# Performance work log

Measured on AMD Instinct MI355X. Metric: run time of the kernel, lower is better.

## Reference

```python
import jax, jax.numpy as jnp
import numpy as np

BETA = 0.5  # exp-sum normalization exponent (not a true softmax)


def setup_inputs() -> dict:
    key = jax.random.key(0)
    ks = jax.random.split(key, 12)
    b, h = 1024, 200
    item_num, region_num, user_num = 50000, 1000, 10000
    d, hid = 128, 128  # embed_size == hidden_size (required by the bmm reshape)
    std = 0.01
    return {
        "history": jax.random.randint(ks[0], (1, b, h), 0, item_num),
        "target": jax.random.randint(ks[1], (1, b), 0, item_num),
        "history_region": jax.random.randint(ks[2], (1, b, h), 0, region_num),
        "target_region": jax.random.randint(ks[3], (1, b), 0, region_num),
        "history_visit_rate": jax.random.uniform(ks[4], (1, h), dtype=jnp.float32),
        "dist_mat": jax.random.uniform(ks[5], (b, h), dtype=jnp.float32),
        "uid": 7,
        "embed_target": std * jax.random.normal(ks[6], (item_num, d // 2), dtype=jnp.float32),
        "embed_region": std * jax.random.normal(ks[7], (region_num, d // 2), dtype=jnp.float32),
        "embed_dist": std * jax.random.normal(ks[8], (user_num, region_num), dtype=jnp.float32),
        "Wq": jax.random.normal(ks[9], (hid, d), dtype=jnp.float32) * (1.0 / np.sqrt(d)),
        "Wk": jax.random.normal(ks[10], (hid, d), dtype=jnp.float32) * (1.0 / np.sqrt(d)),
        "Wv": jax.random.normal(ks[11], (d, d), dtype=jnp.float32) * (1.0 / np.sqrt(d)),
    }


def reference(history, target, history_region, target_region, history_visit_rate,
              dist_mat, uid, embed_target, embed_region, embed_dist, Wq, Wk, Wv):
    h_idx = history[0]            # [b, h]
    tgt = target[0]               # [b]
    hr = history_region[0]        # [b, h]
    tr = target_region[0]         # [b]
    hv = history_visit_rate[0]    # [h]
    b, hlen = h_idx.shape

    # embedding gathers + concat (target half | region half)
    hist_emb = jnp.concatenate([embed_target[h_idx], embed_region[hr]], axis=-1)  # [b,h,d]
    tgt_emb = jnp.concatenate([embed_target[tgt], embed_region[tr]], axis=-1)     # [b,d]
    hd = embed_dist[uid][hr]      # [b, h]
    td = embed_dist[uid][tr]      # [b]
    d = tgt_emb.shape[1]

    # QKV projections (torch Linear: y = x @ W.T)
    q = tgt_emb @ Wq.T            # [b, d]  (hidden == d)
    k = hist_emb @ Wk.T           # [b, h, d]
    v = hist_emb @ Wv.T           # [b, h, d]

    # faithful to original: key reshaped (NOT transposed) to [b, d, h]
    k_r = k.reshape(b, d, hlen)
    scores = jnp.einsum('bd,bdh->bh', q, k_r) / jnp.sqrt(jnp.float32(d))  # [b,h]

    # exp / beta-normalized attention with equality mask
    mask = (h_idx != tgt[:, None]).astype(scores.dtype)
    exp_A = jnp.exp(scores) * mask                          # [b,h]
    exp_sum = jnp.sum(exp_A, axis=-1) ** BETA               # [b]
    attn = exp_A / exp_sum[:, None]                         # [b,h]

    # geo weights: td @ hd is a vector-matrix product -> [h], broadcast over b
    geo = jnp.exp(-1.0 / (jax.nn.relu(td @ hd) + 1.0) * dist_mat)  # [b,h]

    result1 = v * (attn + geo)[..., None]                   # [b,h,d]
    result2 = hist_emb * jnp.broadcast_to(hv, (b, hlen))[..., None]
    result = result1 + result2                              # [b,h,d]

    pred = jnp.einsum('bhd,bd->b', result, tgt_emb)         # bmm + sum over h
    return jax.nn.sigmoid(pred)
```

## Files before the change

kernel.cpp:

```cpp
#include <hip/hip_runtime.h>

typedef unsigned short USH;
typedef unsigned int   UIN;
typedef unsigned char  UCH;

static constexpr int Bn = 1024;
static constexpr int Hn = 200;
static constexpr int Dn = 128;
static constexpr int Dh = 64;
static constexpr int NITEM = 50000;
static constexpr int NREG  = 1000;
static constexpr int MT = 64;
static constexpr int AB_A_BLOCKS = (NITEM + MT - 1) / MT;
static constexpr int AB_B_BLOCKS = (NREG  + MT - 1) / MT;
static constexpr int AB_TOT = AB_A_BLOCKS + AB_B_BLOCKS;
static constexpr int QU_BLOCKS = Bn / 4;
static constexpr int G_BLOCKS  = Bn / 16;
static constexpr int WTS = 132;
static constexpr int ETS = 69;
static constexpr int CR  = 50;
static constexpr int RS  = 192;

static constexpr float FSCALE = 128.f;
static constexpr float FINV   = 1.f / 128.f;

__device__ __forceinline__ float bf2f(USH u) {
  return __uint_as_float(((UIN)u) << 16);
}
__device__ __forceinline__ USH f2b(float f) {
  UIN x = __float_as_uint(f);
  return (USH)((x + 0x7fffu + ((x >> 16) & 1u)) >> 16);
}
__device__ __forceinline__ UIN enc4(float a, float b, float c, float d) {
  int w = __builtin_amdgcn_cvt_pk_fp8_f32(a, b, 0, false);
  w = __builtin_amdgcn_cvt_pk_fp8_f32(c, d, w, true);
  return (UIN)w;
}
__device__ __forceinline__ void dec4(UIN w, float* o) {
  auto lo = __builtin_amdgcn_cvt_pk_f32_fp8((int)w, false);
  auto hi = __builtin_amdgcn_cvt_pk_f32_fp8((int)w, true);
  o[0] = lo[0]; o[1] = lo[1]; o[2] = hi[0]; o[3] = hi[1];
}

__global__ __launch_bounds__(256, 2) void ab_kernel(
    const float* __restrict__ Et, const float* __restrict__ Er,
    const float* __restrict__ Wk, const float* __restrict__ Wq,
    const float* __restrict__ Wv, const int* __restrict__ target,
    const int* __restrict__ tregion, const int* __restrict__ hregion,
    const float* __restrict__ embed_dist, const int* __restrict__ uid,
    UCH* __restrict__ Cf, UCH* __restrict__ Df,
    float* __restrict__ qvt, float* __restrict__ uvt, float* __restrict__ g) {
  __shared__ float wt[64 * WTS];
  __shared__ float et[MT * ETS];
  int blk = blockIdx.x, tid = threadIdx.x;

  if (blk >= AB_TOT + QU_BLOCKS) {
    int c = tid;
    const float* row = embed_dist + (size_t)uid[0] * NREG;
    float acc = 0.f;
    int ibase = (blk - AB_TOT - QU_BLOCKS) * 16;
    for (int ii = 0; ii < 16; ii++) {
      int i = ibase + ii;
      float td = row[tregion[i]];
      if (c < Hn) acc += td * row[hregion[(size_t)i * Hn + c]];
    }
    if (c < Hn) atomicAdd(&g[c], acc);
    return;
  }

  if (blk >= AB_TOT) {
    float* te = wt;
    int i0 = (blk - AB_TOT) * 4;
#pragma unroll
    for (int v = 0; v < 2; v++) {
      int idx = v * 256 + tid;
      int ii = idx >> 7, d = idx & 127;
      int it = i0 + ii;
      te[ii * 128 + d] = (d < 64) ? Et[(size_t)target[it] * Dh + d]
                                  : Er[(size_t)tregion[it] * Dh + (d - 64)];
    }
    __syncthreads();
    int j = tid & 127, half = tid >> 7;
    float a0 = 0.f, a1 = 0.f, a2 = 0.f, a3 = 0.f;
    if (half == 0) {
      const float* wr = Wq + (size_t)j * Dn;
#pragma unroll 8
      for (int k = 0; k < 128; k++) {
        float w = wr[k];
        a0 += w * te[k]; a1 += w * te[128 + k];
        a2 += w * te[256 + k]; a3 += w * te[384 + k];
      }
      const float s = 0.088388347648318447f;
      qvt[(size_t)(i0 + 0) * Dn + j] = a0 * s;
      qvt[(size_t)(i0 + 1) * Dn + j] = a1 * s;
      qvt[(size_t)(i0 + 2) * Dn + j] = a2 * s;
      qvt[(size_t)(i0 + 3) * Dn + j] = a3 * s;
    } else {
      int d = j;
#pragma unroll 8
      for (int k = 0; k < 128; k++) {
        float w = Wv[(size_t)k * Dn + d];
        a0 += w * te[k]; a1 += w * te[128 + k];
        a2 += w * te[256 + k]; a3 += w * te[384 + k];
      }
      uvt[(size_t)(i0 + 0) * Dn + d] = a0;
      uvt[(size_t)(i0 + 1) * Dn + d] = a1;
      uvt[(size_t)(i0 + 2) * Dn + d] = a2;
      uvt[(size_t)(i0 + 3) * Dn + d] = a3;
    }
    return;
  }

  const float* E; UCH* OutT; int nmax, base, koff;
  if (blk < AB_A_BLOCKS) { E = Et; OutT = Cf; nmax = NITEM; base = blk * MT; koff = 0; }
  else { E = Er; OutT = Df; nmax = NREG; base = (blk - AB_A_BLOCKS) * MT; koff = 64; }

#pragma unroll
  for (int p = 0; p < 8; p++) {
    int idx = p * 256 + tid;
    int row = idx >> 4, c4 = idx & 15;
    float4 w = *reinterpret_cast<const float4*>(Wk + (size_t)row * Dn + koff + c4 * 4);
    wt[(c4 * 4 + 0) * WTS + row] = w.x;
    wt[(c4 * 4 + 1) * WTS + row] = w.y;
    wt[(c4 * 4 + 2) * WTS + row] = w.z;
    wt[(c4 * 4 + 3) * WTS + row] = w.w;
  }
#pragma unroll
  for (int p = 0; p < 4; p++) {
    int idx = p * 256 + tid;
    int m = idx >> 4, c4 = idx & 15;
    int gi = base + m;
    float4 e = make_float4(0.f, 0.f, 0.f, 0.f);
    if (gi < nmax) e = *reinterpret_cast<const float4*>(E + (size_t)gi * Dh + c4 * 4);
    et[m * ETS + c4 * 4 + 0] = e.x;
    et[m * ETS + c4 * 4 + 1] = e.y;
    et[m * ETS + c4 * 4 + 2] = e.z;
    et[m * ETS + c4 * 4 + 3] = e.w;
  }
  __syncthreads();

#pragma unroll
  for (int p = 0; p < 4; p++) {
    int idx = p * 256 + tid;
    int m = idx >> 4, wr = idx & 15;
    int gi = base + m;
    if (gi < nmax) {
      const float* er = &et[m * ETS + wr * 4];
      *reinterpret_cast<UIN*>(OutT + (size_t)gi * RS + 128 + wr * 4) =
          enc4(er[0] * FSCALE, er[1] * FSCALE, er[2] * FSCALE, er[3] * FSCALE);
    }
  }

  int jt = tid & 15, it = tid >> 4;
  const float* wb = wt + jt * 8;
  const float* eb = et + (it * 4) * ETS;
  float c[4][8];
#pragma unroll
  for (int ii = 0; ii < 4; ii++)
#pragma unroll
    for (int jj = 0; jj < 8; jj++) c[ii][jj] = 0.f;

#pragma unroll 2
  for (int k = 0; k < 64; k++) {
    float4 w0 = *reinterpret_cast<const float4*>(wb + (size_t)k * WTS);
    float4 w1 = *reinterpret_cast<const float4*>(wb + (size_t)k * WTS + 4);
    float e0 = eb[k], e1 = eb[ETS + k], e2 = eb[2 * ETS + k], e3 = eb[3 * ETS + k];
    c[0][0] += e0 * w0.x; c[0][1] += e0 * w0.y; c[0][2] += e0 * w0.z; c[0][3] += e0 * w0.w;
    c[0][4] += e0 * w1.x; c[0][5] += e0 * w1.y; c[0][6] += e0 * w1.z; c[0][7] += e0 * w1.w;
    c[1][0] += e1 * w0.x; c[1][1] += e1 * w0.y; c[1][2] += e1 * w0.z; c[1][3] += e1 * w0.w;
    c[1][4] += e1 * w1.x; c[1][5] += e1 * w1.y; c[1][6] += e1 * w1.z; c[1][7] += e1 * w1.w;
    c[2][0] += e2 * w0.x; c[2][1] += e2 * w0.y; c[2][2] += e2 * w0.z; c[2][3] += e2 * w0.w;
    c[2][4] += e2 * w1.x; c[2][5] += e2 * w1.y; c[2][6] += e2 * w1.z; c[2][7] += e2 * w1.w;
    c[3][0] += e3 * w0.x; c[3][1] += e3 * w0.y; c[3][2] += e3 * w0.z; c[3][3] += e3 * w0.w;
    c[3][4] += e3 * w1.x; c[3][5] += e3 * w1.y; c[3][6] += e3 * w1.z; c[3][7] += e3 * w1.w;
  }

#pragma unroll
  for (int ii = 0; ii < 4; ii++) {
    int item = base + it * 4 + ii;
    if (item < nmax) {
      uint2 pk;
      pk.x = enc4(c[ii][0] * FSCALE, c[ii][1] * FSCALE, c[ii][2] * FSCALE, c[ii][3] * FSCALE);
      pk.y = enc4(c[ii][4] * FSCALE, c[ii][5] * FSCALE, c[ii][6] * FSCALE, c[ii][7] * FSCALE);
      *reinterpret_cast<uint2*>(OutT + (size_t)item * RS + jt * 8) = pk;
    }
  }
}

__global__ __launch_bounds__(256, 6) void sc_kernel(
    const int* __restrict__ history, const int* __restrict__ target,
    const int* __restrict__ hregion, const int* __restrict__ tregion,
    const float* __restrict__ Et, const float* __restrict__ Er,
    const float* __restrict__ qvt, const float* __restrict__ uvt,
    const UCH* __restrict__ Cf, const UCH* __restrict__ Df,
    float* __restrict__ psc, float2* __restrict__ s12) {
  __shared__ USH kvs[CR * Dn];
  __shared__ uint4 rawA[CR * 4];
  __shared__ uint4 rawB[CR * 4];
  __shared__ float tgtE[128], uvf[128], qv[32];
  int b = blockIdx.x, i = b >> 2, h = b & 3;
  int tid = threadIdx.x;
  const int* hrow = history + (size_t)i * Hn + CR * h;
  const int* rrow = hregion + (size_t)i * Hn + CR * h;

  if (tid < 128) {
    tgtE[tid] = FINV * ((tid < 64) ? Et[(size_t)target[i] * Dh + tid]
                                   : Er[(size_t)tregion[i] * Dh + (tid - 64)]);
  } else {
    uvf[tid - 128] = FINV * uvt[(size_t)i * Dn + (tid - 128)];
  }
  if (tid < 32) qv[tid] = FINV * qvt[(size_t)i * Dn + 32 * h + tid];

  {
    int seg = tid & 3, row = tid >> 2;
    if (row < CR) {
      int ia = hrow[row], ib = rrow[row];
      rawA[row * 4 + seg] = *reinterpret_cast<const uint4*>(Cf + (size_t)ia * RS + 128 + seg * 16);
      rawB[row * 4 + seg] = *reinterpret_cast<const uint4*>(Df + (size_t)ib * RS + 128 + seg * 16);
    }
  }

#pragma unroll
  for (int p = 0; p < 2; p++) {
    int idx = p * 256 + tid;
    int seg = idx & 7, row = idx >> 3;
    if (row < CR) {
      int ia = hrow[row], ib = rrow[row];
      uint4 av = *reinterpret_cast<const uint4*>(Cf + (size_t)ia * RS + seg * 16);
      uint4 bv = *reinterpret_cast<const uint4*>(Df + (size_t)ib * RS + seg * 16);
      float fa[16], fb[16];
      dec4(av.x, fa);      dec4(av.y, fa + 4);  dec4(av.z, fa + 8);  dec4(av.w, fa + 12);
      dec4(bv.x, fb);      dec4(bv.y, fb + 4);  dec4(bv.z, fb + 8);  dec4(bv.w, fb + 12);
      uint4 k0, k1;
      k0.x = (UIN)f2b(fa[0] + fb[0])  | ((UIN)f2b(fa[1] + fb[1]) << 16);
      k0.y = (UIN)f2b(fa[2] + fb[2])  | ((UIN)f2b(fa[3] + fb[3]) << 16);
      k0.z = (UIN)f2b(fa[4] + fb[4])  | ((UIN)f2b(fa[5] + fb[5]) << 16);
      k0.w = (UIN)f2b(fa[6] + fb[6])  | ((UIN)f2b(fa[7] + fb[7]) << 16);
      k1.x = (UIN)f2b(fa[8] + fb[8])  | ((UIN)f2b(fa[9] + fb[9]) << 16);
      k1.y = (UIN)f2b(fa[10] + fb[10]) | ((UIN)f2b(fa[11] + fb[11]) << 16);
      k1.z = (UIN)f2b(fa[12] + fb[12]) | ((UIN)f2b(fa[13] + fb[13]) << 16);
      k1.w = (UIN)f2b(fa[14] + fb[14]) | ((UIN)f2b(fa[15] + fb[15]) << 16);
      *reinterpret_cast<uint4*>(&kvs[row * Dn + seg * 16]) = k0;
      *reinterpret_cast<uint4*>(&kvs[row * Dn + seg * 16 + 8]) = k1;
    }
  }
  __syncthreads();

  int l8 = tid & 7, r8 = tid >> 3;
#pragma unroll
  for (int pass = 0; pass < 2; pass++) {
    int t = (pass == 0) ? r8 : 32 + r8;
    if (t < CR) {
      uint2 e = *(reinterpret_cast<const uint2*>(&rawA[t * 4]) + l8);
      uint2 r = *(reinterpret_cast<const uint2*>(&rawB[t * 4]) + l8);
      float fe[8], fr[8];
      dec4(e.x, fe); dec4(e.y, fe + 4);
      dec4(r.x, fr); dec4(r.y, fr + 4);
      const float* u0 = &uvf[l8 * 8];       const float* t0 = &tgtE[l8 * 8];
      const float* u1 = &uvf[64 + l8 * 8];  const float* t1 = &tgtE[64 + l8 * 8];
      float s1a = fe[0] * u0[0] + fe[1] * u0[1] + fe[2] * u0[2] + fe[3] * u0[3]
                + fe[4] * u0[4] + fe[5] * u0[5] + fe[6] * u0[6] + fe[7] * u0[7]
                + fr[0] * u1[0] + fr[1] * u1[1] + fr[2] * u1[2] + fr[3] * u1[3]
                + fr[4] * u1[4] + fr[5] * u1[5] + fr[6] * u1[6] + fr[7] * u1[7];
      float s2a = fe[0] * t0[0] + fe[1] * t0[1] + fe[2] * t0[2] + fe[3] * t0[3]
                + fe[4] * t0[4] + fe[5] * t0[5] + fe[6] * t0[6] + fe[7] * t0[7]
                + fr[0] * t1[0] + fr[1] * t1[1] + fr[2] * t1[2] + fr[3] * t1[3]
                + fr[4] * t1[4] + fr[5] * t1[5] + fr[6] * t1[6] + fr[7] * t1[7];
      s1a += __shfl_xor(s1a, 1, 64); s2a += __shfl_xor(s2a, 1, 64);
      s1a += __shfl_xor(s1a, 2, 64); s2a += __shfl_xor(s2a, 2, 64);
      s1a += __shfl_xor(s1a, 4, 64); s2a += __shfl_xor(s2a, 4, 64);
      if (l8 == 0) s12[(size_t)i * Hn + CR * h + t] = make_float2(s1a, s2a);
    }
  }

  if (tid < Hn) {
    float acc = 0.f;
    const USH* kp = &kvs[tid];
#pragma unroll
    for (int a = 0; a < 32; a++) acc += qv[a] * bf2f(kp[a * 200]);
    psc[((size_t)i * 4 + h) * Hn + tid] = acc;
  }
}

__global__ __launch_bounds__(256, 8) void ep_kernel(
    const int* __restrict__ history, const int* __restrict__ target,
    const float* __restrict__ hv, const float* __restrict__ dist_mat,
    const float* __restrict__ g, const float* __restrict__ psc,
    const float2* __restrict__ s12, float* __restrict__ out) {
  __shared__ float red[8];
  int i = blockIdx.x, tid = threadIdx.x, lane = tid & 63, wave = tid >> 6;
  int tgt_i = target[i];

  float ea = 0.f; float2 sv = make_float2(0.f, 0.f);
  if (tid < Hn) {
    const float* pp = psc + (size_t)i * 4 * Hn + tid;
    float s = (pp[0] + pp[Hn]) + (pp[2 * Hn] + pp[3 * Hn]);
    sv = s12[(size_t)i * Hn + tid];
    ea = (history[(size_t)i * Hn + tid] != tgt_i) ? __expf(s) : 0.f;
  }
  float wsum = ea;
  for (int off = 32; off > 0; off >>= 1) wsum += __shfl_down(wsum, off, 64);
  if (lane == 0) red[wave] = wsum;
  __syncthreads();
  float esum = red[0] + red[1] + red[2] + red[3];
  float inv = esum > 0.f ? 1.f / sqrtf(esum) : 0.f;

  float part = 0.f;
  if (tid < Hn) {
    float gc = g[tid]; gc = gc > 0.f ? gc : 0.f;
    float dm = dist_mat[(size_t)i * Hn + tid];
    float geo = __expf(-dm / (gc + 1.f));
    part = (ea * inv + geo) * sv.x + hv[tid] * sv.y;
  }
  __syncthreads();
  for (int off = 32; off > 0; off >>= 1) part += __shfl_down(part, off, 64);
  if (lane == 0) red[wave] = part;
  __syncthreads();
  if (tid == 0) {
    float pred = red[0] + red[1] + red[2] + red[3];
    out[i] = 1.f / (1.f + __expf(-pred));
  }
}

extern "C" void kernel_launch(void* const* d_in, const int* in_sizes, int n_in,
                              void* d_out, int out_size, void* d_ws, size_t ws_size,
                              hipStream_t stream) {
  const int*   history = (const int*)d_in[0];
  const int*   target  = (const int*)d_in[1];
  const int*   hregion = (const int*)d_in[2];
  const int*   tregion = (const int*)d_in[3];
  const float* hv      = (const float*)d_in[4];
  const float* dist    = (const float*)d_in[5];
  const int*   uid     = (const int*)d_in[6];
  const float* Et      = (const float*)d_in[7];
  const float* Er      = (const float*)d_in[8];
  const float* Edist   = (const float*)d_in[9];
  const float* Wq      = (const float*)d_in[10];
  const float* Wk      = (const float*)d_in[11];
  const float* Wv      = (const float*)d_in[12];

  char* w = (char*)d_ws;
  float* g   = (float*)w;
  UCH*   Cf  = (UCH*)(w + 1024);
  UCH*   Df  = Cf + (size_t)NITEM * RS;
  float* qvt = (float*)(Df + (size_t)NREG * RS);
  float* uvt = qvt + (size_t)Bn * Dn;
  float* psc = uvt + (size_t)Bn * Dn;
  float2* s12 = (float2*)(psc + (size_t)Bn * 4 * Hn);
  float* out = (float*)d_out;

  hipMemsetAsync(g, 0, Hn * sizeof(float), stream);
  ab_kernel<<<AB_TOT + QU_BLOCKS + G_BLOCKS, 256, 0, stream>>>(
      Et, Er, Wk, Wq, Wv, target, tregion, hregion, Edist, uid,
      Cf, Df, qvt, uvt, g);
  sc_kernel<<<Bn * 4, 256, 0, stream>>>(history, target, hregion, tregion,
                                        Et, Er, qvt, uvt, Cf, Df, psc, s12);
  ep_kernel<<<Bn, 256, 0, stream>>>(history, target, hv, dist, g, psc, s12, out);
}
```

Before: 152.2 us.

## Fuse three kernels into one persistent cooperative kernel with grid syncs

Merges the projection/table-building, scoring, and epilogue kernels into one cooperative persistent kernel. Each block loops over virtual block indices, and grid.sync() separates the phases. The aim is to drop two kernel launch gaps and their tail effects. In exchange, the grid is capped at occupancy times 256 CUs, shared memory is sized for the largest phase (which may limit occupancy in later phases), and grid-wide barriers add their own cost.

New measurement: 291.6 us. 1.92x slower.

```diff
diff --git a/kernel.cpp b/kernel.cpp
--- a/kernel.cpp
+++ b/kernel.cpp
@@ -1,4 +1,7 @@
 #include <hip/hip_runtime.h>
+#include <hip/hip_cooperative_groups.h>
+
+namespace cg = cooperative_groups;
 
 typedef unsigned short USH;
 typedef unsigned int   UIN;
@@ -20,6 +23,7 @@
 static constexpr int ETS = 69;
 static constexpr int CR  = 50;
 static constexpr int RS  = 192;
+static constexpr int VIRT_A = AB_TOT + QU_BLOCKS + G_BLOCKS;
 
 static constexpr float FSCALE = 128.f;
 static constexpr float FINV   = 1.f / 128.f;
@@ -42,283 +46,290 @@
   o[0] = lo[0]; o[1] = lo[1]; o[2] = hi[0]; o[3] = hi[1];
 }
 
-__global__ __launch_bounds__(256, 2) void ab_kernel(
+__global__ __launch_bounds__(256, 3) void mega_kernel(
+    const int* __restrict__ history, const int* __restrict__ target,
+    const int* __restrict__ hregion, const int* __restrict__ tregion,
+    const float* __restrict__ hv, const float* __restrict__ dist_mat,
+    const int* __restrict__ uid,
     const float* __restrict__ Et, const float* __restrict__ Er,
-    const float* __restrict__ Wk, const float* __restrict__ Wq,
-    const float* __restrict__ Wv, const int* __restrict__ target,
-    const int* __restrict__ tregion, const int* __restrict__ hregion,
-    const float* __restrict__ embed_dist, const int* __restrict__ uid,
+    const float* __restrict__ embed_dist,
+    const float* __restrict__ Wq, const float* __restrict__ Wk,
+    const float* __restrict__ Wv,
     UCH* __restrict__ Cf, UCH* __restrict__ Df,
-    float* __restrict__ qvt, float* __restrict__ uvt, float* __restrict__ g) {
-  __shared__ float wt[64 * WTS];
-  __shared__ float et[MT * ETS];
-  int blk = blockIdx.x, tid = threadIdx.x;
-
-  if (blk >= AB_TOT + QU_BLOCKS) {
-    int c = tid;
-    const float* row = embed_dist + (size_t)uid[0] * NREG;
-    float acc = 0.f;
-    int ibase = (blk - AB_TOT - QU_BLOCKS) * 16;
-    for (int ii = 0; ii < 16; ii++) {
-      int i = ibase + ii;
-      float td = row[tregion[i]];
-      if (c < Hn) acc += td * row[hregion[(size_t)i * Hn + c]];
-    }
-    if (c < Hn) atomicAdd(&g[c], acc);
-    return;
-  }
-
-  if (blk >= AB_TOT) {
-    float* te = wt;
-    int i0 = (blk - AB_TOT) * 4;
-#pragma unroll
-    for (int v = 0; v < 2; v++) {
-      int idx = v * 256 + tid;
-      int ii = idx >> 7, d = idx & 127;
-      int it = i0 + ii;
-      te[ii * 128 + d] = (d < 64) ? Et[(size_t)target[it] * Dh + d]
-                                  : Er[(size_t)tregion[it] * Dh + (d - 64)];
-    }
-    __syncthreads();
-    int j = tid & 127, half = tid >> 7;
-    float a0 = 0.f, a1 = 0.f, a2 = 0.f, a3 = 0.f;
-    if (half == 0) {
-      const float* wr = Wq + (size_t)j * Dn;
+    float* __restrict__ qvt, float* __restrict__ uvt, float* __restrict__ g,
+    float* __restrict__ psc, float2* __restrict__ s12,
+    float* __restrict__ out) {
+  __shared__ float smem[64 * WTS + 64 * ETS];
+  int tid = threadIdx.x;
+  cg::grid_group grid = cg::this_grid();
+
+  {
+    float* wt = smem;
+    float* et = smem + 64 * WTS;
+    for (int blk = blockIdx.x; blk < VIRT_A; blk += gridDim.x) {
+      __syncthreads();
+      if (blk >= AB_TOT + QU_BLOCKS) {
+        int c = tid;
+        const float* row = embed_dist + (size_t)uid[0] * NREG;
+        float acc = 0.f;
+        int ibase = (blk - AB_TOT - QU_BLOCKS) * 16;
+        for (int ii = 0; ii < 16; ii++) {
+          int i = ibase + ii;
+          float td = row[tregion[i]];
+          if (c < Hn) acc += td * row[hregion[(size_t)i * Hn + c]];
+        }
+        if (c < Hn) atomicAdd(&g[c], acc);
+      } else if (blk >= AB_TOT) {
+        float* te = wt;
+        int i0 = (blk - AB_TOT) * 4;
+#pragma unroll
+        for (int v = 0; v < 2; v++) {
+          int idx = v * 256 + tid;
+          int ii = idx >> 7, d = idx & 127;
+          int it = i0 + ii;
+          te[ii * 128 + d] = (d < 64) ? Et[(size_t)target[it] * Dh + d]
+                                      : Er[(size_t)tregion[it] * Dh + (d - 64)];
+        }
+        __syncthreads();
+        int j = tid & 127, half = tid >> 7;
+        float a0 = 0.f, a1 = 0.f, a2 = 0.f, a3 = 0.f;
+        if (half == 0) {
+          const float* wr = Wq + (size_t)j * Dn;
 #pragma unroll 8
-      for (int k = 0; k < 128; k++) {
-        float w = wr[k];
-        a0 += w * te[k]; a1 += w * te[128 + k];
-        a2 += w * te[256 + k]; a3 += w * te[384 + k];
-      }
-      const float s = 0.088388347648318447f;
-      qvt[(size_t)(i0 + 0) * Dn + j] = a0 * s;
-      qvt[(size_t)(i0 + 1) * Dn + j] = a1 * s;
-      qvt[(size_t)(i0 + 2) * Dn + j] = a2 * s;
-      qvt[(size_t)(i0 + 3) * Dn + j] = a3 * s;
-    } else {
-      int d = j;
+          for (int k = 0; k < 128; k++) {
+            float w = wr[k];
+            a0 += w * te[k]; a1 += w * te[128 + k];
+            a2 += w * te[256 + k]; a3 += w * te[384 + k];
+          }
+          const float s = 0.088388347648318447f;
+          qvt[(size_t)(i0 + 0) * Dn + j] = a0 * s;
+          qvt[(size_t)(i0 + 1) * Dn + j] = a1 * s;
+          qvt[(size_t)(i0 + 2) * Dn + j] = a2 * s;
+          qvt[(size_t)(i0 + 3) * Dn + j] = a3 * s;
+        } else {
+          int d = j;
 #pragma unroll 8
-      for (int k = 0; k < 128; k++) {
-        float w = Wv[(size_t)k * Dn + d];
-        a0 += w * te[k]; a1 += w * te[128 + k];
-        a2 += w * te[256 + k]; a3 += w * te[384 + k];
-      }
-      uvt[(size_t)(i0 + 0) * Dn + d] = a0;
-      uvt[(size_t)(i0 + 1) * Dn + d] = a1;
-      uvt[(size_t)(i0 + 2) * Dn + d] = a2;
-      uvt[(size_t)(i0 + 3) * Dn + d] = a3;
-    }
-    return;
-  }
-
-  const float* E; UCH* OutT; int nmax, base, koff;
-  if (blk < AB_A_BLOCKS) { E = Et; OutT = Cf; nmax = NITEM; base = blk * MT; koff = 0; }
-  else { E = Er; OutT = Df; nmax = NREG; base = (blk - AB_A_BLOCKS) * MT; koff = 64; }
-
-#pragma unroll
-  for (int p = 0; p < 8; p++) {
-    int idx = p * 256 + tid;
-    int row = idx >> 4, c4 = idx & 15;
-    float4 w = *reinterpret_cast<const float4*>(Wk + (size_t)row * Dn + koff + c4 * 4);
-    wt[(c4 * 4 + 0) * WTS + row] = w.x;
-    wt[(c4 * 4 + 1) * WTS + row] = w.y;
-    wt[(c4 * 4 + 2) * WTS + row] = w.z;
-    wt[(c4 * 4 + 3) * WTS + row] = w.w;
-  }
-#pragma unroll
-  for (int p = 0; p < 4; p++) {
-    int idx = p * 256 + tid;
-    int m = idx >> 4, c4 = idx & 15;
-    int gi = base + m;
-    float4 e = make_float4(0.f, 0.f, 0.f, 0.f);
-    if (gi < nmax) e = *reinterpret_cast<const float4*>(E + (size_t)gi * Dh + c4 * 4);
-    et[m * ETS + c4 * 4 + 0] = e.x;
-    et[m * ETS + c4 * 4 + 1] = e.y;
-    et[m * ETS + c4 * 4 + 2] = e.z;
-    et[m * ETS + c4 * 4 + 3] = e.w;
-  }
-  __syncthreads();
-
-#pragma unroll
-  for (int p = 0; p < 4; p++) {
-    int idx = p * 256 + tid;
-    int m = idx >> 4, wr = idx & 15;
-    int gi = base + m;
-    if (gi < nmax) {
-      const float* er = &et[m * ETS + wr * 4];
-      *reinterpret_cast<UIN*>(OutT + (size_t)gi * RS + 128 + wr * 4) =
-          enc4(er[0] * FSCALE, er[1] * FSCALE, er[2] * FSCALE, er[3] * FSCALE);
+          for (int k = 0; k < 128; k++) {
+            float w = Wv[(size_t)k * Dn + d];
+            a0 += w * te[k]; a1 += w * te[128 + k];
+            a2 += w * te[256 + k]; a3 += w * te[384 + k];
+          }
+          uvt[(size_t)(i0 + 0) * Dn + d] = a0;
+          uvt[(size_t)(i0 + 1) * Dn + d] = a1;
+          uvt[(size_t)(i0 + 2) * Dn + d] = a2;
+          uvt[(size_t)(i0 + 3) * Dn + d] = a3;
+        }
+      } else {
+        const float* E; UCH* OutT; int nmax, base, koff;
+        if (blk < AB_A_BLOCKS) { E = Et; OutT = Cf; nmax = NITEM; base = blk * MT; koff = 0; }
+        else { E = Er; OutT = Df; nmax = NREG; base = (blk - AB_A_BLOCKS) * MT; koff = 64; }
+
+#pragma unroll
+        for (int p = 0; p < 8; p++) {
+          int idx = p * 256 + tid;
+          int row = idx >> 4, c4 = idx & 15;
+          float4 w = *reinterpret_cast<const float4*>(Wk + (size_t)row * Dn + koff + c4 * 4);
+          wt[(c4 * 4 + 0) * WTS + row] = w.x;
+          wt[(c4 * 4 + 1) * WTS + row] = w.y;
+          wt[(c4 * 4 + 2) * WTS + row] = w.z;
+          wt[(c4 * 4 + 3) * WTS + row] = w.w;
+        }
+#pragma unroll
+        for (int p = 0; p < 4; p++) {
+          int idx = p * 256 + tid;
+          int m = idx >> 4, c4 = idx & 15;
+          int gi = base + m;
+          float4 e = make_float4(0.f, 0.f, 0.f, 0.f);
+          if (gi < nmax) e = *reinterpret_cast<const float4*>(E + (size_t)gi * Dh + c4 * 4);
+          et[m * ETS + c4 * 4 + 0] = e.x;
+          et[m * ETS + c4 * 4 + 1] = e.y;
+          et[m * ETS + c4 * 4 + 2] = e.z;
+          et[m * ETS + c4 * 4 + 3] = e.w;
+        }
+        __syncthreads();
+
+#pragma unroll
+        for (int p = 0; p < 4; p++) {
+          int idx = p * 256 + tid;
+          int m = idx >> 4, wr = idx & 15;
+          int gi = base + m;
+          if (gi < nmax) {
+            const float* er = &et[m * ETS + wr * 4];
+            *reinterpret_cast<UIN*>(OutT + (size_t)gi * RS + 128 + wr * 4) =
+                enc4(er[0] * FSCALE, er[1] * FSCALE, er[2] * FSCALE, er[3] * FSCALE);
+          }
+        }
+
+        int jt = tid & 15, it = tid >> 4;
+        const float* wb = wt + jt * 8;
+        const float* eb = et + (it * 4) * ETS;
+        float c[4][8];
+#pragma unroll
+        for (int ii = 0; ii < 4; ii++)
+#pragma unroll
+          for (int jj = 0; jj < 8; jj++) c[ii][jj] = 0.f;
+
+#pragma unroll 2
+        for (int k = 0; k < 64; k++) {
+          float4 w0 = *reinterpret_cast<const float4*>(wb + (size_t)k * WTS);
+          float4 w1 = *reinterpret_cast<const float4*>(wb + (size_t)k * WTS + 4);
+          float e0 = eb[k], e1 = eb[ETS + k], e2 = eb[2 * ETS + k], e3 = eb[3 * ETS + k];
+          c[0][0] += e0 * w0.x; c[0][1] += e0 * w0.y; c[0][2] += e0 * w0.z; c[0][3] += e0 * w0.w;
+          c[0][4] += e0 * w1.x; c[0][5] += e0 * w1.y; c[0][6] += e0 * w1.z; c[0][7] += e0 * w1.w;
+          c[1][0] += e1 * w0.x; c[1][1] += e1 * w0.y; c[1][2] += e1 * w0.z; c[1][3] += e1 * w0.w;
+          c[1][4] += e1 * w1.x; c[1][5] += e1 * w1.y; c[1][6] += e1 * w1.z; c[1][7] += e1 * w1.w;
+          c[2][0] += e2 * w0.x; c[2][1] += e2 * w0.y; c[2][2] += e2 * w0.z; c[2][3] += e2 * w0.w;
+          c[2][4] += e2 * w1.x; c[2][5] += e2 * w1.y; c[2][6] += e2 * w1.z; c[2][7] += e2 * w1.w;
+          c[3][0] += e3 * w0.x; c[3][1] += e3 * w0.y; c[3][2] += e3 * w0.z; c[3][3] += e3 * w0.w;
+          c[3][4] += e3 * w1.x; c[3][5] += e3 * w1.y; c[3][6] += e3 * w1.z; c[3][7] += e3 * w1.w;
+        }
+
+#pragma unroll
+        for (int ii = 0; ii < 4; ii++) {
+          int item = base + it * 4 + ii;
+          if (item < nmax) {
+            uint2 pk;
+            pk.x = enc4(c[ii][0] * FSCALE, c[ii][1] * FSCALE, c[ii][2] * FSCALE, c[ii][3] * FSCALE);
+            pk.y = enc4(c[ii][4] * FSCALE, c[ii][5] * FSCALE, c[ii][6] * FSCALE, c[ii][7] * FSCALE);
+            *reinterpret_cast<uint2*>(OutT + (size_t)item * RS + jt * 8) = pk;
+          }
+        }
+      }
     }
   }
-
-  int jt = tid & 15, it = tid >> 4;
-  const float* wb = wt + jt * 8;
-  const float* eb = et + (it * 4) * ETS;
-  float c[4][8];
-#pragma unroll
-  for (int ii = 0; ii < 4; ii++)
-#pragma unroll
-    for (int jj = 0; jj < 8; jj++) c[ii][jj] = 0.f;
-
-#pragma unroll 2
-  for (int k = 0; k < 64; k++) {
-    float4 w0 = *reinterpret_cast<const float4*>(wb + (size_t)k * WTS);
-    float4 w1 = *reinterpret_cast<const float4*>(wb + (size_t)k * WTS + 4);
-    float e0 = eb[k], e1 = eb[ETS + k], e2 = eb[2 * ETS + k], e3 = eb[3 * ETS + k];
-    c[0][0] += e0 * w0.x; c[0][1] += e0 * w0.y; c[0][2] += e0 * w0.z; c[0][3] += e0 * w0.w;
-    c[0][4] += e0 * w1.x; c[0][5] += e0 * w1.y; c[0][6] += e0 * w1.z; c[0][7] += e0 * w1.w;
-    c[1][0] += e1 * w0.x; c[1][1] += e1 * w0.y; c[1][2] += e1 * w0.z; c[1][3] += e1 * w0.w;
-    c[1][4] += e1 * w1.x; c[1][5] += e1 * w1.y; c[1][6] += e1 * w1.z; c[1][7] += e1 * w1.w;
-    c[2][0] += e2 * w0.x; c[2][1] += e2 * w0.y; c[2][2] += e2 * w0.z; c[2][3] += e2 * w0.w;
-    c[2][4] += e2 * w1.x; c[2][5] += e2 * w1.y; c[2][6] += e2 * w1.z; c[2][7] += e2 * w1.w;
-    c[3][0] += e3 * w0.x; c[3][1] += e3 * w0.y; c[3][2] += e3 * w0.z; c[3][3] += e3 * w0.w;
-    c[3][4] += e3 * w1.x; c[3][5] += e3 * w1.y; c[3][6] += e3 * w1.z; c[3][7] += e3 * w1.w;
-  }
-
-#pragma unroll
-  for (int ii = 0; ii < 4; ii++) {
-    int item = base + it * 4 + ii;
-    if (item < nmax) {
-      uint2 pk;
-      pk.x = enc4(c[ii][0] * FSCALE, c[ii][1] * FSCALE, c[ii][2] * FSCALE, c[ii][3] * FSCALE);
-      pk.y = enc4(c[ii][4] * FSCALE, c[ii][5] * FSCALE, c[ii][6] * FSCALE, c[ii][7] * FSCALE);
-      *reinterpret_cast<uint2*>(OutT + (size_t)item * RS + jt * 8) = pk;
+  grid.sync();
+
+  {
+    USH*   kvs  = (USH*)smem;
+    uint4* rawA = (uint4*)(smem + 3200);
+    uint4* rawB = (uint4*)(smem + 4000);
+    float* tgtE = smem + 4800;
+    float* uvf  = smem + 4928;
+    float* qv   = smem + 5056;
+    for (int vb = blockIdx.x; vb < Bn * 4; vb += gridDim.x) {
+      __syncthreads();
+      int i = vb >> 2, h = vb & 3;
+      const int* hrow = history + (size_t)i * Hn + CR * h;
+      const int* rrow = hregion + (size_t)i * Hn + CR * h;
+
+      if (tid < 128) {
+        tgtE[tid] = FINV * ((tid < 64) ? Et[(size_t)target[i] * Dh + tid]
+                                       : Er[(size_t)tregion[i] * Dh + (tid - 64)]);
+      } else {
+        uvf[tid - 128] = FINV * uvt[(size_t)i * Dn + (tid - 128)];
+      }
+      if (tid < 32) qv[tid] = FINV * qvt[(size_t)i * Dn + 32 * h + tid];
+
+      {
+        int seg = tid & 3, row = tid >> 2;
+        if (row < CR) {
+          int ia = hrow[row], ib = rrow[row];
+          rawA[row * 4 + seg] = *reinterpret_cast<const uint4*>(Cf + (size_t)ia * RS + 128 + seg * 16);
+          rawB[row * 4 + seg] = *reinterpret_cast<const uint4*>(Df + (size_t)ib * RS + 128 + seg * 16);
+        }
+      }
+
+#pragma unroll
+      for (int p = 0; p < 2; p++) {
+        int idx = p * 256 + tid;
+        int seg = idx & 7, row = idx >> 3;
+        if (row < CR) {
+          int ia = hrow[row], ib = rrow[row];
+          uint4 av = *reinterpret_cast<const uint4*>(Cf + (size_t)ia * RS + seg * 16);
+          uint4 bv = *reinterpret_cast<const uint4*>(Df + (size_t)ib * RS + seg * 16);
+          float fa[16], fb[16];
+          dec4(av.x, fa);      dec4(av.y, fa + 4);  dec4(av.z, fa + 8);  dec4(av.w, fa + 12);
+          dec4(bv.x, fb);      dec4(bv.y, fb + 4);  dec4(bv.z, fb + 8);  dec4(bv.w, fb + 12);
+          uint4 k0, k1;
+          k0.x = (UIN)f2b(fa[0] + fb[0])  | ((UIN)f2b(fa[1] + fb[1]) << 16);
+          k0.y = (UIN)f2b(fa[2] + fb[2])  | ((UIN)f2b(fa[3] + fb[3]) << 16);
+          k0.z = (UIN)f2b(fa[4] + fb[4])  | ((UIN)f2b(fa[5] + fb[5]) << 16);
+          k0.w = (UIN)f2b(fa[6] + fb[6])  | ((UIN)f2b(fa[7] + fb[7]) << 16);
+          k1.x = (UIN)f2b(fa[8] + fb[8])  | ((UIN)f2b(fa[9] + fb[9]) << 16);
+          k1.y = (UIN)f2b(fa[10] + fb[10]) | ((UIN)f2b(fa[11] + fb[11]) << 16);
+          k1.z = (UIN)f2b(fa[12] + fb[12]) | ((UIN)f2b(fa[13] + fb[13]) << 16);
+          k1.w = (UIN)f2b(fa[14] + fb[14]) | ((UIN)f2b(fa[15] + fb[15]) << 16);
+          *reinterpret_cast<uint4*>(&kvs[row * Dn + seg * 16]) = k0;
+          *reinterpret_cast<uint4*>(&kvs[row * Dn + seg * 16 + 8]) = k1;
+        }
+      }
+      __syncthreads();
+
+      int l8 = tid & 7, r8 = tid >> 3;
+#pragma unroll
+      for (int pass = 0; pass < 2; pass++) {
+        int t = (pass == 0) ? r8 : 32 + r8;
+        if (t < CR) {
+          uint2 e = *(reinterpret_cast<const uint2*>(&rawA[t * 4]) + l8);
+          uint2 r = *(reinterpret_cast<const uint2*>(&rawB[t * 4]) + l8);
+          float fe[8], fr[8];
+          dec4(e.x, fe); dec4(e.y, fe + 4);
+          dec4(r.x, fr); dec4(r.y, fr + 4);
+          const float* u0 = &uvf[l8 * 8];       const float* t0 = &tgtE[l8 * 8];
+          const float* u1 = &uvf[64 + l8 * 8];  const float* t1 = &tgtE[64 + l8 * 8];
+          float s1a = fe[0] * u0[0] + fe[1] * u0[1] + fe[2] * u0[2] + fe[3] * u0[3]
+                    + fe[4] * u0[4] + fe[5] * u0[5] + fe[6] * u0[6] + fe[7] * u0[7]
+                    + fr[0] * u1[0] + fr[1] * u1[1] + fr[2] * u1[2] + fr[3] * u1[3]
+                    + fr[4] * u1[4] + fr[5] * u1[5] + fr[6] * u1[6] + fr[7] * u1[7];
+          float s2a = fe[0] * t0[0] + fe[1] * t0[1] + fe[2] * t0[2] + fe[3] * t0[3]
+                    + fe[4] * t0[4] + fe[5] * t0[5] + fe[6] * t0[6] + fe[7] * t0[7]
+                    + fr[0] * t1[0] + fr[1] * t1[1] + fr[2] * t1[2] + fr[3] * t1[3]
+                    + fr[4] * t1[4] + fr[5] * t1[5] + fr[6] * t1[6] + fr[7] * t1[7];
+          s1a += __shfl_xor(s1a, 1, 64); s2a += __shfl_xor(s2a, 1, 64);
+          s1a += __shfl_xor(s1a, 2, 64); s2a += __shfl_xor(s2a, 2, 64);
+          s1a += __shfl_xor(s1a, 4, 64); s2a += __shfl_xor(s2a, 4, 64);
+          if (l8 == 0) s12[(size_t)i * Hn + CR * h + t] = make_float2(s1a, s2a);
+        }
+      }
+
+      if (tid < Hn) {
+        float acc = 0.f;
+        const USH* kp = &kvs[tid];
+#pragma unroll
+        for (int a = 0; a < 32; a++) acc += qv[a] * bf2f(kp[a * 200]);
+        psc[((size_t)i * 4 + h) * Hn + tid] = acc;
+      }
     }
   }
-}
-
-__global__ __launch_bounds__(256, 6) void sc_kernel(
-    const int* __restrict__ history, const int* __restrict__ target,
-    const int* __restrict__ hregion, const int* __restrict__ tregion,
-    const float* __restrict__ Et, const float* __restrict__ Er,
-    const float* __restrict__ qvt, const float* __restrict__ uvt,
-    const UCH* __restrict__ Cf, const UCH* __restrict__ Df,
-    float* __restrict__ psc, float2* __restrict__ s12) {
-  __shared__ USH kvs[CR * Dn];
-  __shared__ uint4 rawA[CR * 4];
-  __shared__ uint4 rawB[CR * 4];
-  __shared__ float tgtE[128], uvf[128], qv[32];
-  int b = blockIdx.x, i = b >> 2, h = b & 3;
-  int tid = threadIdx.x;
-  const int* hrow = history + (size_t)i * Hn + CR * h;
-  const int* rrow = hregion + (size_t)i * Hn + CR * h;
-
-  if (tid < 128) {
-    tgtE[tid] = FINV * ((tid < 64) ? Et[(size_t)target[i] * Dh + tid]
-                                   : Er[(size_t)tregion[i] * Dh + (tid - 64)]);
-  } else {
-    uvf[tid - 128] = FINV * uvt[(size_t)i * Dn + (tid - 128)];
-  }
-  if (tid < 32) qv[tid] = FINV * qvt[(size_t)i * Dn + 32 * h + tid];
+  grid.sync();
 
   {
-    int seg = tid & 3, row = tid >> 2;
-    if (row < CR) {
-      int ia = hrow[row], ib = rrow[row];
-      rawA[row * 4 + seg] = *reinterpret_cast<const uint4*>(Cf + (size_t)ia * RS + 128 + seg * 16);
-      rawB[row * 4 + seg] = *reinterpret_cast<const uint4*>(Df + (size_t)ib * RS + 128 + seg * 16);
+    float* red = smem;
+    int lane = tid & 63, wave = tid >> 6;
+    for (int i = blockIdx.x; i < Bn; i += gridDim.x) {
+      __syncthreads();
+      int tgt_i = target[i];
+
+      float ea = 0.f; float2 sv = make_float2(0.f, 0.f);
+      if (tid < Hn) {
+        const float* pp = psc + (size_t)i * 4 * Hn + tid;
+        float s = (pp[0] + pp[Hn]) + (pp[2 * Hn] + pp[3 * Hn]);
+        sv = s12[(size_t)i * Hn + tid];
+        ea = (history[(size_t)i * Hn + tid] != tgt_i) ? __expf(s) : 0.f;
+      }
+      float wsum = ea;
+      for (int off = 32; off > 0; off >>= 1) wsum += __shfl_down(wsum, off, 64);
+      if (lane == 0) red[wave] = wsum;
+      __syncthreads();
+      float esum = red[0] + red[1] + red[2] + red[3];
+      float inv = esum > 0.f ? 1.f / sqrtf(esum) : 0.f;
+
+      float part = 0.f;
+      if (tid < Hn) {
+        float gc = g[tid]; gc = gc > 0.f ? gc : 0.f;
+        float dm = dist_mat[(size_t)i * Hn + tid];
+        float geo = __expf(-dm / (gc + 1.f));
+        part = (ea * inv + geo) * sv.x + hv[tid] * sv.y;
+      }
+      __syncthreads();
+      for (int off = 32; off > 0; off >>= 1) part += __shfl_down(part, off, 64);
+      if (lane == 0) red[wave] = part;
+      __syncthreads();
+      if (tid == 0) {
+        float pred = red[0] + red[1] + red[2] + red[3];
+        out[i] = 1.f / (1.f + __expf(-pred));
+      }
     }
-  }
-
-#pragma unroll
-  for (int p = 0; p < 2; p++) {
-    int idx = p * 256 + tid;
-    int seg = idx & 7, row = idx >> 3;
-    if (row < CR) {
-      int ia = hrow[row], ib = rrow[row];
-      uint4 av = *reinterpret_cast<const uint4*>(Cf + (size_t)ia * RS + seg * 16);
-      uint4 bv = *reinterpret_cast<const uint4*>(Df + (size_t)ib * RS + seg * 16);
-      float fa[16], fb[16];
-      dec4(av.x, fa);      dec4(av.y, fa + 4);  dec4(av.z, fa + 8);  dec4(av.w, fa + 12);
-      dec4(bv.x, fb);      dec4(bv.y, fb + 4);  dec4(bv.z, fb + 8);  dec4(bv.w, fb + 12);
-      uint4 k0, k1;
-      k0.x = (UIN)f2b(fa[0] + fb[0])  | ((UIN)f2b(fa[1] + fb[1]) << 16);
-      k0.y = (UIN)f2b(fa[2] + fb[2])  | ((UIN)f2b(fa[3] + fb[3]) << 16);
-      k0.z = (UIN)f2b(fa[4] + fb[4])  | ((UIN)f2b(fa[5] + fb[5]) << 16);
-      k0.w = (UIN)f2b(fa[6] + fb[6])  | ((UIN)f2b(fa[7] + fb[7]) << 16);
-      k1.x = (UIN)f2b(fa[8] + fb[8])  | ((UIN)f2b(fa[9] + fb[9]) << 16);
-      k1.y = (UIN)f2b(fa[10] + fb[10]) | ((UIN)f2b(fa[11] + fb[11]) << 16);
-      k1.z = (UIN)f2b(fa[12] + fb[12]) | ((UIN)f2b(fa[13] + fb[13]) << 16);
-      k1.w = (UIN)f2b(fa[14] + fb[14]) | ((UIN)f2b(fa[15] + fb[15]) << 16);
-      *reinterpret_cast<uint4*>(&kvs[row * Dn + seg * 16]) = k0;
-      *reinterpret_cast<uint4*>(&kvs[row * Dn + seg * 16 + 8]) = k1;
-    }
-  }
-  __syncthreads();
-
-  int l8 = tid & 7, r8 = tid >> 3;
-#pragma unroll
-  for (int pass = 0; pass < 2; pass++) {
-    int t = (pass == 0) ? r8 : 32 + r8;
-    if (t < CR) {
-      uint2 e = *(reinterpret_cast<const uint2*>(&rawA[t * 4]) + l8);
-      uint2 r = *(reinterpret_cast<const uint2*>(&rawB[t * 4]) + l8);
-      float fe[8], fr[8];
-      dec4(e.x, fe); dec4(e.y, fe + 4);
-      dec4(r.x, fr); dec4(r.y, fr + 4);
-      const float* u0 = &uvf[l8 * 8];       const float* t0 = &tgtE[l8 * 8];
-      const float* u1 = &uvf[64 + l8 * 8];  const float* t1 = &tgtE[64 + l8 * 8];
-      float s1a = fe[0] * u0[0] + fe[1] * u0[1] + fe[2] * u0[2] + fe[3] * u0[3]
-                + fe[4] * u0[4] + fe[5] * u0[5] + fe[6] * u0[6] + fe[7] * u0[7]
-                + fr[0] * u1[0] + fr[1] * u1[1] + fr[2] * u1[2] + fr[3] * u1[3]
-                + fr[4] * u1[4] + fr[5] * u1[5] + fr[6] * u1[6] + fr[7] * u1[7];
-      float s2a = fe[0] * t0[0] + fe[1] * t0[1] + fe[2] * t0[2] + fe[3] * t0[3]
-                + fe[4] * t0[4] + fe[5] * t0[5] + fe[6] * t0[6] + fe[7] * t0[7]
-                + fr[0] * t1[0] + fr[1] * t1[1] + fr[2] * t1[2] + fr[3] * t1[3]
-                + fr[4] * t1[4] + fr[5] * t1[5] + fr[6] * t1[6] + fr[7] * t1[7];
-      s1a += __shfl_xor(s1a, 1, 64); s2a += __shfl_xor(s2a, 1, 64);
-      s1a += __shfl_xor(s1a, 2, 64); s2a += __shfl_xor(s2a, 2, 64);
-      s1a += __shfl_xor(s1a, 4, 64); s2a += __shfl_xor(s2a, 4, 64);
-      if (l8 == 0) s12[(size_t)i * Hn + CR * h + t] = make_float2(s1a, s2a);
-    }
-  }
-
-  if (tid < Hn) {
-    float acc = 0.f;
-    const USH* kp = &kvs[tid];
-#pragma unroll
-    for (int a = 0; a < 32; a++) acc += qv[a] * bf2f(kp[a * 200]);
-    psc[((size_t)i * 4 + h) * Hn + tid] = acc;
-  }
-}
-
-__global__ __launch_bounds__(256, 8) void ep_kernel(
-    const int* __restrict__ history, const int* __restrict__ target,
-    const float* __restrict__ hv, const float* __restrict__ dist_mat,
-    const float* __restrict__ g, const float* __restrict__ psc,
-    const float2* __restrict__ s12, float* __restrict__ out) {
-  __shared__ float red[8];
-  int i = blockIdx.x, tid = threadIdx.x, lane = tid & 63, wave = tid >> 6;
-  int tgt_i = target[i];
-
-  float ea = 0.f; float2 sv = make_float2(0.f, 0.f);
-  if (tid < Hn) {
-    const float* pp = psc + (size_t)i * 4 * Hn + tid;
-    float s = (pp[0] + pp[Hn]) + (pp[2 * Hn] + pp[3 * Hn]);
-    sv = s12[(size_t)i * Hn + tid];
-    ea = (history[(size_t)i * Hn + tid] != tgt_i) ? __expf(s) : 0.f;
-  }
-  float wsum = ea;
-  for (int off = 32; off > 0; off >>= 1) wsum += __shfl_down(wsum, off, 64);
-  if (lane == 0) red[wave] = wsum;
-  __syncthreads();
-  float esum = red[0] + red[1] + red[2] + red[3];
-  float inv = esum > 0.f ? 1.f / sqrtf(esum) : 0.f;
-
-  float part = 0.f;
-  if (tid < Hn) {
-    float gc = g[tid]; gc = gc > 0.f ? gc : 0.f;
-    float dm = dist_mat[(size_t)i * Hn + tid];
-    float geo = __expf(-dm / (gc + 1.f));
-    part = (ea * inv + geo) * sv.x + hv[tid] * sv.y;
-  }
-  __syncthreads();
-  for (int off = 32; off > 0; off >>= 1) part += __shfl_down(part, off, 64);
-  if (lane == 0) red[wave] = part;
-  __syncthreads();
-  if (tid == 0) {
-    float pred = red[0] + red[1] + red[2] + red[3];
-    out[i] = 1.f / (1.f + __expf(-pred));
   }
 }
 
@@ -350,10 +361,20 @@
   float* out = (float*)d_out;
 
   hipMemsetAsync(g, 0, Hn * sizeof(float), stream);
-  ab_kernel<<<AB_TOT + QU_BLOCKS + G_BLOCKS, 256, 0, stream>>>(
-      Et, Er, Wk, Wq, Wv, target, tregion, hregion, Edist, uid,
-      Cf, Df, qvt, uvt, g);
-  sc_kernel<<<Bn * 4, 256, 0, stream>>>(history, target, hregion, tregion,
-                                        Et, Er, qvt, uvt, Cf, Df, psc, s12);
-  ep_kernel<<<Bn, 256, 0, stream>>>(history, target, hv, dist, g, psc, s12, out);
-}
+
+  int maxb = 0;
+  if (hipOccupancyMaxActiveBlocksPerMultiprocessor(&maxb, mega_kernel, 256, 0) != hipSuccess || maxb < 1)
+    maxb = 3;
+  int nblk = maxb * 256;
+  if (nblk > 4096) nblk = 4096;
+
+  void* args[] = {
+      (void*)&history, (void*)&target, (void*)&hregion, (void*)&tregion,
+      (void*)&hv, (void*)&dist, (void*)&uid,
+      (void*)&Et, (void*)&Er, (void*)&Edist,
+      (void*)&Wq, (void*)&Wk, (void*)&Wv,
+      (void*)&Cf, (void*)&Df, (void*)&qvt, (void*)&uvt, (void*)&g,
+      (void*)&psc, (void*)&s12, (void*)&out};
+  hipLaunchCooperativeKernel(reinterpret_cast<const void*>(mega_kernel),
+                             dim3(nblk), dim3(256), args, 0, stream);
+}
```

## Fuse score and epilogue kernels into one per-batch block

Applied to the files above, without the earlier changes.

Merges the score kernel and the epilogue kernel into a single kernel where each block handles one batch row and loops over the four history chunks. Partial scores and s1/s2 dot products stay in shared memory instead of being written to and read back from global scratch, and one kernel launch is removed. In exchange the grid shrinks fourfold and the chunks are processed serially with barriers, reducing parallelism and latency hiding for the gathers.

New measurement: 150.9 us. About the same (-0.8%).

```diff
diff --git a/kernel.cpp b/kernel.cpp
--- a/kernel.cpp
+++ b/kernel.cpp
@@ -187,116 +187,116 @@
   }
 }
 
-__global__ __launch_bounds__(256, 6) void sc_kernel(
+__global__ __launch_bounds__(256, 4) void scep_kernel(
     const int* __restrict__ history, const int* __restrict__ target,
     const int* __restrict__ hregion, const int* __restrict__ tregion,
     const float* __restrict__ Et, const float* __restrict__ Er,
     const float* __restrict__ qvt, const float* __restrict__ uvt,
     const UCH* __restrict__ Cf, const UCH* __restrict__ Df,
-    float* __restrict__ psc, float2* __restrict__ s12) {
+    const float* __restrict__ hv, const float* __restrict__ dist_mat,
+    const float* __restrict__ g, float* __restrict__ out) {
   __shared__ USH kvs[CR * Dn];
   __shared__ uint4 rawA[CR * 4];
   __shared__ uint4 rawB[CR * 4];
   __shared__ float tgtE[128], uvf[128], qv[32];
-  int b = blockIdx.x, i = b >> 2, h = b & 3;
-  int tid = threadIdx.x;
-  const int* hrow = history + (size_t)i * Hn + CR * h;
-  const int* rrow = hregion + (size_t)i * Hn + CR * h;
-
-  if (tid < 128) {
-    tgtE[tid] = FINV * ((tid < 64) ? Et[(size_t)target[i] * Dh + tid]
-                                   : Er[(size_t)tregion[i] * Dh + (tid - 64)]);
-  } else {
-    uvf[tid - 128] = FINV * uvt[(size_t)i * Dn + (tid - 128)];
-  }
-  if (tid < 32) qv[tid] = FINV * qvt[(size_t)i * Dn + 32 * h + tid];
-
-  {
-    int seg = tid & 3, row = tid >> 2;
-    if (row < CR) {
-      int ia = hrow[row], ib = rrow[row];
-      rawA[row * 4 + seg] = *reinterpret_cast<const uint4*>(Cf + (size_t)ia * RS + 128 + seg * 16);
-      rawB[row * 4 + seg] = *reinterpret_cast<const uint4*>(Df + (size_t)ib * RS + 128 + seg * 16);
-    }
-  }
-
-#pragma unroll
-  for (int p = 0; p < 2; p++) {
-    int idx = p * 256 + tid;
-    int seg = idx & 7, row = idx >> 3;
-    if (row < CR) {
-      int ia = hrow[row], ib = rrow[row];
-      uint4 av = *reinterpret_cast<const uint4*>(Cf + (size_t)ia * RS + seg * 16);
-      uint4 bv = *reinterpret_cast<const uint4*>(Df + (size_t)ib * RS + seg * 16);
-      float fa[16], fb[16];
-      dec4(av.x, fa);      dec4(av.y, fa + 4);  dec4(av.z, fa + 8);  dec4(av.w, fa + 12);
-      dec4(bv.x, fb);      dec4(bv.y, fb + 4);  dec4(bv.z, fb + 8);  dec4(bv.w, fb + 12);
-      uint4 k0, k1;
-      k0.x = (UIN)f2b(fa[0] + fb[0])  | ((UIN)f2b(fa[1] + fb[1]) << 16);
-      k0.y = (UIN)f2b(fa[2] + fb[2])  | ((UIN)f2b(fa[3] + fb[3]) << 16);
-      k0.z = (UIN)f2b(fa[4] + fb[4])  | ((UIN)f2b(fa[5] + fb[5]) << 16);
-      k0.w = (UIN)f2b(fa[6] + fb[6])  | ((UIN)f2b(fa[7] + fb[7]) << 16);
-      k1.x = (UIN)f2b(fa[8] + fb[8])  | ((UIN)f2b(fa[9] + fb[9]) << 16);
-      k1.y = (UIN)f2b(fa[10] + fb[10]) | ((UIN)f2b(fa[11] + fb[11]) << 16);
-      k1.z = (UIN)f2b(fa[12] + fb[12]) | ((UIN)f2b(fa[13] + fb[13]) << 16);
-      k1.w = (UIN)f2b(fa[14] + fb[14]) | ((UIN)f2b(fa[15] + fb[15]) << 16);
-      *reinterpret_cast<uint4*>(&kvs[row * Dn + seg * 16]) = k0;
-      *reinterpret_cast<uint4*>(&kvs[row * Dn + seg * 16 + 8]) = k1;
-    }
-  }
-  __syncthreads();
-
-  int l8 = tid & 7, r8 = tid >> 3;
-#pragma unroll
-  for (int pass = 0; pass < 2; pass++) {
-    int t = (pass == 0) ? r8 : 32 + r8;
-    if (t < CR) {
-      uint2 e = *(reinterpret_cast<const uint2*>(&rawA[t * 4]) + l8);
-      uint2 r = *(reinterpret_cast<const uint2*>(&rawB[t * 4]) + l8);
-      float fe[8], fr[8];
-      dec4(e.x, fe); dec4(e.y, fe + 4);
-      dec4(r.x, fr); dec4(r.y, fr + 4);
-      const float* u0 = &uvf[l8 * 8];       const float* t0 = &tgtE[l8 * 8];
-      const float* u1 = &uvf[64 + l8 * 8];  const float* t1 = &tgtE[64 + l8 * 8];
-      float s1a = fe[0] * u0[0] + fe[1] * u0[1] + fe[2] * u0[2] + fe[3] * u0[3]
-                + fe[4] * u0[4] + fe[5] * u0[5] + fe[6] * u0[6] + fe[7] * u0[7]
-                + fr[0] * u1[0] + fr[1] * u1[1] + fr[2] * u1[2] + fr[3] * u1[3]
-                + fr[4] * u1[4] + fr[5] * u1[5] + fr[6] * u1[6] + fr[7] * u1[7];
-      float s2a = fe[0] * t0[0] + fe[1] * t0[1] + fe[2] * t0[2] + fe[3] * t0[3]
-                + fe[4] * t0[4] + fe[5] * t0[5] + fe[6] * t0[6] + fe[7] * t0[7]
-                + fr[0] * t1[0] + fr[1] * t1[1] + fr[2] * t1[2] + fr[3] * t1[3]
-                + fr[4] * t1[4] + fr[5] * t1[5] + fr[6] * t1[6] + fr[7] * t1[7];
-      s1a += __shfl_xor(s1a, 1, 64); s2a += __shfl_xor(s2a, 1, 64);
-      s1a += __shfl_xor(s1a, 2, 64); s2a += __shfl_xor(s2a, 2, 64);
-      s1a += __shfl_xor(s1a, 4, 64); s2a += __shfl_xor(s2a, 4, 64);
-      if (l8 == 0) s12[(size_t)i * Hn + CR * h + t] = make_float2(s1a, s2a);
-    }
-  }
-
-  if (tid < Hn) {
-    float acc = 0.f;
-    const USH* kp = &kvs[tid];
-#pragma unroll
-    for (int a = 0; a < 32; a++) acc += qv[a] * bf2f(kp[a * 200]);
-    psc[((size_t)i * 4 + h) * Hn + tid] = acc;
-  }
-}
-
-__global__ __launch_bounds__(256, 8) void ep_kernel(
-    const int* __restrict__ history, const int* __restrict__ target,
-    const float* __restrict__ hv, const float* __restrict__ dist_mat,
-    const float* __restrict__ g, const float* __restrict__ psc,
-    const float2* __restrict__ s12, float* __restrict__ out) {
+  __shared__ float pacc[Hn];
+  __shared__ float2 s12L[Hn];
   __shared__ float red[8];
-  int i = blockIdx.x, tid = threadIdx.x, lane = tid & 63, wave = tid >> 6;
+  int i = blockIdx.x, tid = threadIdx.x;
   int tgt_i = target[i];
 
+  for (int h = 0; h < 4; h++) {
+    const int* hrow = history + (size_t)i * Hn + CR * h;
+    const int* rrow = hregion + (size_t)i * Hn + CR * h;
+
+    if (h == 0) {
+      if (tid < 128) {
+        tgtE[tid] = FINV * ((tid < 64) ? Et[(size_t)tgt_i * Dh + tid]
+                                       : Er[(size_t)tregion[i] * Dh + (tid - 64)]);
+      } else {
+        uvf[tid - 128] = FINV * uvt[(size_t)i * Dn + (tid - 128)];
+      }
+      if (tid < Hn) pacc[tid] = 0.f;
+    }
+    if (tid < 32) qv[tid] = FINV * qvt[(size_t)i * Dn + 32 * h + tid];
+
+    {
+      int seg = tid & 3, row = tid >> 2;
+      if (row < CR) {
+        int ia = hrow[row], ib = rrow[row];
+        rawA[row * 4 + seg] = *reinterpret_cast<const uint4*>(Cf + (size_t)ia * RS + 128 + seg * 16);
+        rawB[row * 4 + seg] = *reinterpret_cast<const uint4*>(Df + (size_t)ib * RS + 128 + seg * 16);
+      }
+    }
+
+#pragma unroll
+    for (int p = 0; p < 2; p++) {
+      int idx = p * 256 + tid;
+      int seg = idx & 7, row = idx >> 3;
+      if (row < CR) {
+        int ia = hrow[row], ib = rrow[row];
+        uint4 av = *reinterpret_cast<const uint4*>(Cf + (size_t)ia * RS + seg * 16);
+        uint4 bv = *reinterpret_cast<const uint4*>(Df + (size_t)ib * RS + seg * 16);
+        float fa[16], fb[16];
+        dec4(av.x, fa);      dec4(av.y, fa + 4);  dec4(av.z, fa + 8);  dec4(av.w, fa + 12);
+        dec4(bv.x, fb);      dec4(bv.y, fb + 4);  dec4(bv.z, fb + 8);  dec4(bv.w, fb + 12);
+        uint4 k0, k1;
+        k0.x = (UIN)f2b(fa[0] + fb[0])  | ((UIN)f2b(fa[1] + fb[1]) << 16);
+        k0.y = (UIN)f2b(fa[2] + fb[2])  | ((UIN)f2b(fa[3] + fb[3]) << 16);
+        k0.z = (UIN)f2b(fa[4] + fb[4])  | ((UIN)f2b(fa[5] + fb[5]) << 16);
+        k0.w = (UIN)f2b(fa[6] + fb[6])  | ((UIN)f2b(fa[7] + fb[7]) << 16);
+        k1.x = (UIN)f2b(fa[8] + fb[8])  | ((UIN)f2b(fa[9] + fb[9]) << 16);
+        k1.y = (UIN)f2b(fa[10] + fb[10]) | ((UIN)f2b(fa[11] + fb[11]) << 16);
+        k1.z = (UIN)f2b(fa[12] + fb[12]) | ((UIN)f2b(fa[13] + fb[13]) << 16);
+        k1.w = (UIN)f2b(fa[14] + fb[14]) | ((UIN)f2b(fa[15] + fb[15]) << 16);
+        *reinterpret_cast<uint4*>(&kvs[row * Dn + seg * 16]) = k0;
+        *reinterpret_cast<uint4*>(&kvs[row * Dn + seg * 16 + 8]) = k1;
+      }
+    }
+    __syncthreads();
+
+    int l8 = tid & 7, r8 = tid >> 3;
+#pragma unroll
+    for (int pass = 0; pass < 2; pass++) {
+      int t = (pass == 0) ? r8 : 32 + r8;
+      if (t < CR) {
+        uint2 e = *(reinterpret_cast<const uint2*>(&rawA[t * 4]) + l8);
+        uint2 r = *(reinterpret_cast<const uint2*>(&rawB[t * 4]) + l8);
+        float fe[8], fr[8];
+        dec4(e.x, fe); dec4(e.y, fe + 4);
+        dec4(r.x, fr); dec4(r.y, fr + 4);
+        const float* u0 = &uvf[l8 * 8];       const float* t0 = &tgtE[l8 * 8];
+        const float* u1 = &uvf[64 + l8 * 8];  const float* t1 = &tgtE[64 + l8 * 8];
+        float s1a = fe[0] * u0[0] + fe[1] * u0[1] + fe[2] * u0[2] + fe[3] * u0[3]
+                  + fe[4] * u0[4] + fe[5] * u0[5] + fe[6] * u0[6] + fe[7] * u0[7]
+                  + fr[0] * u1[0] + fr[1] * u1[1] + fr[2] * u1[2] + fr[3] * u1[3]
+                  + fr[4] * u1[4] + fr[5] * u1[5] + fr[6] * u1[6] + fr[7] * u1[7];
+        float s2a = fe[0] * t0[0] + fe[1] * t0[1] + fe[2] * t0[2] + fe[3] * t0[3]
+                  + fe[4] * t0[4] + fe[5] * t0[5] + fe[6] * t0[6] + fe[7] * t0[7]
+                  + fr[0] * t1[0] + fr[1] * t1[1] + fr[2] * t1[2] + fr[3] * t1[3]
+                  + fr[4] * t1[4] + fr[5] * t1[5] + fr[6] * t1[6] + fr[7] * t1[7];
+        s1a += __shfl_xor(s1a, 1, 64); s2a += __shfl_xor(s2a, 1, 64);
+        s1a += __shfl_xor(s1a, 2, 64); s2a += __shfl_xor(s2a, 2, 64);
+        s1a += __shfl_xor(s1a, 4, 64); s2a += __shfl_xor(s2a, 4, 64);
+        if (l8 == 0) s12L[CR * h + t] = make_float2(s1a, s2a);
+      }
+    }
+
+    if (tid < Hn) {
+      float acc = 0.f;
+      const USH* kp = &kvs[tid];
+#pragma unroll
+      for (int a = 0; a < 32; a++) acc += qv[a] * bf2f(kp[a * 200]);
+      pacc[tid] += acc;
+    }
+    __syncthreads();
+  }
+
+  int lane = tid & 63, wave = tid >> 6;
   float ea = 0.f; float2 sv = make_float2(0.f, 0.f);
   if (tid < Hn) {
-    const float* pp = psc + (size_t)i * 4 * Hn + tid;
-    float s = (pp[0] + pp[Hn]) + (pp[2 * Hn] + pp[3 * Hn]);
-    sv = s12[(size_t)i * Hn + tid];
-    ea = (history[(size_t)i * Hn + tid] != tgt_i) ? __expf(s) : 0.f;
+    sv = s12L[tid];
+    ea = (history[(size_t)i * Hn + tid] != tgt_i) ? __expf(pacc[tid]) : 0.f;
   }
   float wsum = ea;
   for (int off = 32; off > 0; off >>= 1) wsum += __shfl_down(wsum, off, 64);
@@ -345,15 +345,13 @@
   UCH*   Df  = Cf + (size_t)NITEM * RS;
   float* qvt = (float*)(Df + (size_t)NREG * RS);
   float* uvt = qvt + (size_t)Bn * Dn;
-  float* psc = uvt + (size_t)Bn * Dn;
-  float2* s12 = (float2*)(psc + (size_t)Bn * 4 * Hn);
   float* out = (float*)d_out;
 
   hipMemsetAsync(g, 0, Hn * sizeof(float), stream);
   ab_kernel<<<AB_TOT + QU_BLOCKS + G_BLOCKS, 256, 0, stream>>>(
       Et, Er, Wk, Wq, Wv, target, tregion, hregion, Edist, uid,
       Cf, Df, qvt, uvt, g);
-  sc_kernel<<<Bn * 4, 256, 0, stream>>>(history, target, hregion, tregion,
-                                        Et, Er, qvt, uvt, Cf, Df, psc, s12);
-  ep_kernel<<<Bn, 256, 0, stream>>>(history, target, hv, dist, g, psc, s12, out);
-}
+  scep_kernel<<<Bn, 256, 0, stream>>>(history, target, hregion, tregion,
+                                      Et, Er, qvt, uvt, Cf, Df,
+                                      hv, dist, g, out);
+}
```
